# Kernel optimization log

Measured on AMD Instinct MI355X. Metric: run time of the kernel, lower is better.

The kernel has to match this reference:

```python
import jax, jax.numpy as jnp
import numpy as np

SIGMA = 0.1
B_PARAM = 1.0
EPS_NORM = 1e-12  # torch F.normalize eps
EPS_MIN = 1e-5


def setup_inputs() -> dict:
    key = jax.random.key(0)
    k1, k2 = jax.random.split(key)
    x = jax.random.normal(k1, (4, 64, 64, 64), dtype=jnp.float32)
    y = jax.random.normal(k2, (4, 64, 64, 64), dtype=jnp.float32)
    return {"x": x, "y": y}


def reference(x, y):
    B, C, H, W = x.shape
    N = H * W
    xf = x.reshape(B, C, N)
    yf = y.reshape(B, C, N)
    # F.normalize along channel dim (L2, eps-clamped denominator)
    xn = xf / jnp.maximum(jnp.linalg.norm(xf, axis=1, keepdims=True), EPS_NORM)
    yn = yf / jnp.maximum(jnp.linalg.norm(yf, axis=1, keepdims=True), EPS_NORM)
    xt = jnp.transpose(xn, (0, 2, 1))  # [B, N, C]
    yt = jnp.transpose(yn, (0, 2, 1))  # [B, N, C]
    x2 = jnp.sum(xt * xt, axis=-1, keepdims=True)          # [B, N, 1]
    y2 = jnp.sum(yt * yt, axis=-1)[:, None, :]             # [B, 1, N]
    d2 = x2 + y2 - 2.0 * jnp.einsum('bnc,bmc->bnm', xt, yt)  # [B, N, N]
    dist = jnp.sqrt(jnp.maximum(d2, 0.0))
    d_min = jnp.min(dist, axis=-1, keepdims=True)
    d_scaled = dist / (d_min + EPS_MIN)
    w = jnp.exp((B_PARAM - d_scaled) / SIGMA)
    cx = w / jnp.sum(w, axis=-1, keepdims=True)
    cx_max = jnp.max(cx, axis=-1)  # [B, N]
    return -jnp.log(jnp.mean(cx_max + EPS_MIN))
```

## Files before the change

kernel.cpp:

```cpp
#include <hip/hip_runtime.h>
#include <math.h>

constexpr int B_   = 4;
constexpr int C_   = 64;
constexpr int HW   = 4096;
constexpr int ROWS = B_ * HW;
constexpr int GRID = 256;

constexpr float SIGMA    = 0.1f;
constexpr float EPS_MIN  = 1e-5f;
constexpr float EPS_NORM = 1e-12f;
constexpr float LOG2E    = 1.44269504088896340736f;

constexpr int XR  = 64;
constexpr int NW  = 16;
constexpr int YW  = HW / NW;
constexpr int SRW = 32;
constexpr int NSW = YW / SRW;

using short8  = __attribute__((ext_vector_type(8))) short;
using floatx4 = __attribute__((ext_vector_type(4))) float;

__device__ inline ushort f2bf(float f) {
    unsigned u = __float_as_uint(f);
    unsigned r = u + 0x7FFFu + ((u >> 16) & 1u);
    return (ushort)(r >> 16);
}

__device__ inline void gload16(const ushort* g, void* lds) {
    __builtin_amdgcn_global_load_lds(
        (const __attribute__((address_space(1))) void*)g,
        (__attribute__((address_space(3))) void*)lds, 16, 0, 0);
}

#define WAIT_VMCNT(n) asm volatile("s_waitcnt vmcnt(" #n ")" ::: "memory")

__global__ __launch_bounds__(256) void nrm_kernel(const float* __restrict__ x,
                                                  const float* __restrict__ y,
                                                  ushort* __restrict__ xn,
                                                  ushort* __restrict__ yn,
                                                  float* __restrict__ total,
                                                  unsigned* __restrict__ cnt) {
    int p = blockIdx.x * 256 + threadIdx.x;
    if (p == 0) { *total = 0.0f; *cnt = 0u; }
    const float* src; ushort* dst; int q; float sgn; bool isy;
    if (p < ROWS) { src = x; dst = xn; q = p; sgn = -2.0f; isy = false; }
    else          { src = y; dst = yn; q = p - ROWS; sgn = 1.0f; isy = true; }
    int b = q >> 12;
    int n = q & (HW - 1);
    const float* base = src + (size_t)(b * C_) * HW + n;
    float v[C_];
    float ss = 0.0f;
#pragma unroll
    for (int c = 0; c < C_; ++c) {
        v[c] = base[(size_t)c * HW];
        ss = fmaf(v[c], v[c], ss);
    }
    float scale = sgn / fmaxf(sqrtf(ss), EPS_NORM);
    short8* o = (short8*)(dst + (size_t)q * C_);
    int sw = isy ? (n & 7) : 0;
#pragma unroll
    for (int c8 = 0; c8 < C_ / 8; ++c8) {
        short8 pk;
#pragma unroll
        for (int j = 0; j < 8; ++j) pk[j] = (short)f2bf(v[c8 * 8 + j] * scale);
        o[c8 ^ sw] = pk;
    }
}

__global__ __launch_bounds__(1024, 4) void main_kernel(const ushort* __restrict__ xn,
                                                       const ushort* __restrict__ yn,
                                                       float* __restrict__ total,
                                                       unsigned* __restrict__ cnt,
                                                       float* __restrict__ out) {
    __shared__ short8 stg[NW][2][SRW * 8];
    __shared__ float  red[NW][XR];
    __shared__ float  dmf[XR];

    const int tid  = threadIdx.x;
    const int wid  = tid >> 6;
    const int lane = tid & 63;
    const int lrow = lane & 15;
    const int kgrp = lane >> 4;

    const int blk   = blockIdx.x;
    const int b     = blk >> 6;
    const int nbase = (blk & 63) * XR;

    const ushort* xb = xn + (size_t)(b * HW + nbase) * C_;
    short8 xf0[4], xf1[4];
#pragma unroll
    for (int xt = 0; xt < 4; ++xt) {
        xf0[xt] = *(const short8*)(xb + (xt * 16 + lrow) * C_ + kgrp * 8);
        xf1[xt] = *(const short8*)(xb + (xt * 16 + lrow) * C_ + 32 + kgrp * 8);
    }

    const ushort* yb = yn + (size_t)(b * HW + wid * YW) * C_ + lane * 8;

#define ISSUE(s, buf) do {                                              \
        const ushort* gp_ = yb + (size_t)(s) * SRW * C_;                \
        _Pragma("unroll")                                               \
        for (int g_ = 0; g_ < 4; ++g_)                                  \
            gload16(gp_ + g_ * 64 * 8, (void*)&stg[wid][buf][g_ * 64]); \
    } while (0)

    float m2[4] = {INFINITY, INFINITY, INFINITY, INFINITY};

    ISSUE(0, 0);
    for (int s = 0; s < NSW; ++s) {
        int cur = s & 1;
        if (s + 1 < NSW) { ISSUE(s + 1, cur ^ 1); WAIT_VMCNT(4); }
        else             { WAIT_VMCNT(0); }
        __builtin_amdgcn_sched_barrier(0);
#pragma unroll
        for (int yt = 0; yt < 2; ++yt) {
            int p = yt * 16 + lrow, q = p & 7;
            short8 ya0 = stg[wid][cur][p * 8 + (kgrp ^ q)];
            short8 ya1 = stg[wid][cur][p * 8 + ((kgrp + 4) ^ q)];
#pragma unroll
            for (int xt = 0; xt < 4; ++xt) {
                floatx4 acc = {2.0f, 2.0f, 2.0f, 2.0f};
                acc = __builtin_amdgcn_mfma_f32_16x16x32_bf16(ya0, xf0[xt], acc, 0, 0, 0);
                acc = __builtin_amdgcn_mfma_f32_16x16x32_bf16(ya1, xf1[xt], acc, 0, 0, 0);
                m2[xt] = fminf(fminf(fminf(acc[0], acc[1]), acc[2]),
                               fminf(acc[3], m2[xt]));
            }
        }
    }

#pragma unroll
    for (int off = 16; off < 64; off <<= 1)
#pragma unroll
        for (int xt = 0; xt < 4; ++xt)
            m2[xt] = fminf(m2[xt], __shfl_xor(m2[xt], off));
    if (kgrp == 0)
#pragma unroll
        for (int xt = 0; xt < 4; ++xt) red[wid][xt * 16 + lrow] = m2[xt];
    __syncthreads();
    if (tid < XR) {
        float m = red[0][tid];
#pragma unroll
        for (int w = 1; w < NW; ++w) m = fminf(m, red[w][tid]);
        dmf[tid] = sqrtf(fmaxf(m, 0.0f));
    }
    __syncthreads();

    float kk2[4], c02[4];
#pragma unroll
    for (int xt = 0; xt < 4; ++xt) {
        float dm = dmf[xt * 16 + lrow];
        kk2[xt] = LOG2E / (SIGMA * (dm + EPS_MIN));
        c02[xt] = dm * kk2[xt];
    }

    float s2[4] = {0.0f, 0.0f, 0.0f, 0.0f};
    ISSUE(0, 0);
    for (int s = 0; s < NSW; ++s) {
        int cur = s & 1;
        if (s + 1 < NSW) { ISSUE(s + 1, cur ^ 1); WAIT_VMCNT(4); }
        else             { WAIT_VMCNT(0); }
        __builtin_amdgcn_sched_barrier(0);
#pragma unroll
        for (int yt = 0; yt < 2; ++yt) {
            int p = yt * 16 + lrow, q = p & 7;
            short8 ya0 = stg[wid][cur][p * 8 + (kgrp ^ q)];
            short8 ya1 = stg[wid][cur][p * 8 + ((kgrp + 4) ^ q)];
#pragma unroll
            for (int xt = 0; xt < 4; ++xt) {
                floatx4 acc = {2.0f, 2.0f, 2.0f, 2.0f};
                acc = __builtin_amdgcn_mfma_f32_16x16x32_bf16(ya0, xf0[xt], acc, 0, 0, 0);
                acc = __builtin_amdgcn_mfma_f32_16x16x32_bf16(ya1, xf1[xt], acc, 0, 0, 0);
                float d0 = __builtin_amdgcn_sqrtf(acc[0]);
                float d1 = __builtin_amdgcn_sqrtf(acc[1]);
                float d2 = __builtin_amdgcn_sqrtf(acc[2]);
                float d3 = __builtin_amdgcn_sqrtf(acc[3]);
                s2[xt] += __builtin_amdgcn_exp2f(fmaf(-kk2[xt], d0, c02[xt]));
                s2[xt] += __builtin_amdgcn_exp2f(fmaf(-kk2[xt], d1, c02[xt]));
                s2[xt] += __builtin_amdgcn_exp2f(fmaf(-kk2[xt], d2, c02[xt]));
                s2[xt] += __builtin_amdgcn_exp2f(fmaf(-kk2[xt], d3, c02[xt]));
            }
        }
    }
#undef ISSUE

#pragma unroll
    for (int off = 16; off < 64; off <<= 1)
#pragma unroll
        for (int xt = 0; xt < 4; ++xt)
            s2[xt] += __shfl_xor(s2[xt], off);
    if (kgrp == 0)
#pragma unroll
        for (int xt = 0; xt < 4; ++xt) red[wid][xt * 16 + lrow] = s2[xt];
    __syncthreads();

    if (tid < 64) {
        float Ssum = (tid < XR) ? red[0][tid] : 0.0f;
        if (tid < XR)
#pragma unroll
            for (int w = 1; w < NW; ++w) Ssum += red[w][tid];
        float acc = (tid < XR) ? (__builtin_amdgcn_rcpf(Ssum) + EPS_MIN) : 0.0f;
#pragma unroll
        for (int off = 32; off > 0; off >>= 1) acc += __shfl_down(acc, off);
        if (tid == 0) {
            atomicAdd(total, acc);
            __threadfence();
            unsigned done = atomicAdd(cnt, 1u);
            if (done == GRID - 1) {
                __threadfence();
                float t = atomicAdd(total, 0.0f);
                out[0] = -logf(t / (float)ROWS);
            }
        }
    }
}

extern "C" void kernel_launch(void* const* d_in, const int* in_sizes, int n_in,
                              void* d_out, int out_size, void* d_ws, size_t ws_size,
                              hipStream_t stream) {
    const float* x = (const float*)d_in[0];
    const float* y = (const float*)d_in[1];
    float* out = (float*)d_out;

    char* ws = (char*)d_ws;
    size_t nrm_bytes = (size_t)ROWS * C_ * sizeof(ushort);
    ushort*   xn    = (ushort*)(ws);
    ushort*   yn    = (ushort*)(ws + nrm_bytes);
    float*    total = (float*)(ws + 2 * nrm_bytes);
    unsigned* cnt   = (unsigned*)(ws + 2 * nrm_bytes + 16);

    hipLaunchKernelGGL(nrm_kernel, dim3(2 * ROWS / 256), dim3(256), 0, stream,
                       x, y, xn, yn, total, cnt);
    hipLaunchKernelGGL(main_kernel, dim3(GRID), dim3(1024), 0, stream,
                       xn, yn, total, cnt, out);
}
```

Before: 95.27 us.

## Split Y range across two blocks per X tile with separate min and sum passes

Each 64-row X tile is now handled by two blocks that each cover half of the Y columns, doubling the grid to 512 blocks. To make that possible the fused kernel is split into a min pass and a sum pass, joined through a global atomicMin array and a global atomicAdd array of per-row sums. The normalize kernel now spreads each row across two threads, and a final last-block reduction computes the loss. This aims to fill more CUs on the GPU, at the cost of two extra launches, global atomics, and a serial 16K-row final reduction in one block.

```diff
diff --git a/kernel.cpp b/kernel.cpp
--- a/kernel.cpp
+++ b/kernel.cpp
@@ -5,18 +5,19 @@
 constexpr int C_   = 64;
 constexpr int HW   = 4096;
 constexpr int ROWS = B_ * HW;
-constexpr int GRID = 256;
 
 constexpr float SIGMA    = 0.1f;
 constexpr float EPS_MIN  = 1e-5f;
 constexpr float EPS_NORM = 1e-12f;
 constexpr float LOG2E    = 1.44269504088896340736f;
 
-constexpr int XR  = 64;
-constexpr int NW  = 16;
-constexpr int YW  = HW / NW;
-constexpr int SRW = 32;
-constexpr int NSW = YW / SRW;
+constexpr int XR   = 64;
+constexpr int YH   = HW / 2;
+constexpr int NW   = 16;
+constexpr int YW   = YH / NW;
+constexpr int SRW  = 16;
+constexpr int NSW  = YW / SRW;
+constexpr int GRID = 512;
 
 using short8  = __attribute__((ext_vector_type(8))) short;
 using floatx4 = __attribute__((ext_vector_type(4))) float;
@@ -39,92 +40,90 @@
                                                   const float* __restrict__ y,
                                                   ushort* __restrict__ xn,
                                                   ushort* __restrict__ yn,
+                                                  unsigned* __restrict__ dmin_u,
                                                   float* __restrict__ total,
                                                   unsigned* __restrict__ cnt) {
-    int p = blockIdx.x * 256 + threadIdx.x;
-    if (p == 0) { *total = 0.0f; *cnt = 0u; }
-    const float* src; ushort* dst; int q; float sgn; bool isy;
-    if (p < ROWS) { src = x; dst = xn; q = p; sgn = -2.0f; isy = false; }
-    else          { src = y; dst = yn; q = p - ROWS; sgn = 1.0f; isy = true; }
+    int T = blockIdx.x * 256 + threadIdx.x;
+    if (T == 0) { *total = 0.0f; *cnt = 0u; }
+    if (T < ROWS) dmin_u[T] = 0x7F800000u;
+    int q = T >> 1;
+    int h = T & 1;
+    const float* src; ushort* dst; float sgn; bool isy;
+    if (q < ROWS) { src = x; dst = xn; sgn = -2.0f; isy = false; }
+    else          { src = y; dst = yn; q -= ROWS; sgn = 1.0f; isy = true; }
     int b = q >> 12;
     int n = q & (HW - 1);
-    const float* base = src + (size_t)(b * C_) * HW + n;
-    float v[C_];
+    const float* base = src + (size_t)(b * C_) * HW + (size_t)(h * 32) * HW + n;
+    float v[32];
     float ss = 0.0f;
 #pragma unroll
-    for (int c = 0; c < C_; ++c) {
-        v[c] = base[(size_t)c * HW];
-        ss = fmaf(v[c], v[c], ss);
-    }
+    for (int j = 0; j < 32; ++j) {
+        v[j] = base[(size_t)j * HW];
+        ss = fmaf(v[j], v[j], ss);
+    }
+    ss += __shfl_xor(ss, 1);
     float scale = sgn / fmaxf(sqrtf(ss), EPS_NORM);
-    short8* o = (short8*)(dst + (size_t)q * C_);
+    short8* orow = (short8*)(dst + (size_t)q * C_);
     int sw = isy ? (n & 7) : 0;
 #pragma unroll
-    for (int c8 = 0; c8 < C_ / 8; ++c8) {
+    for (int j4 = 0; j4 < 4; ++j4) {
         short8 pk;
 #pragma unroll
-        for (int j = 0; j < 8; ++j) pk[j] = (short)f2bf(v[c8 * 8 + j] * scale);
-        o[c8 ^ sw] = pk;
-    }
-}
-
-__global__ __launch_bounds__(1024, 4) void main_kernel(const ushort* __restrict__ xn,
-                                                       const ushort* __restrict__ yn,
-                                                       float* __restrict__ total,
-                                                       unsigned* __restrict__ cnt,
-                                                       float* __restrict__ out) {
+        for (int j = 0; j < 8; ++j) pk[j] = (short)f2bf(v[j4 * 8 + j] * scale);
+        orow[(h * 4 + j4) ^ sw] = pk;
+    }
+}
+
+#define PASS_SETUP                                                          \
+    const int tid  = threadIdx.x;                                           \
+    const int wid  = tid >> 6;                                   \
+    const int lane = tid & 63;                                              \
+    const int lrow = lane & 15;                      \
+    const int kgrp = lane >> 4;                           \
+    const int pairid = blockIdx.x >> 1;                                     \
+    const int half   = blockIdx.x & 1;                                      \
+    const int b      = pairid >> 6;                 \
+    const int nbase  = (pairid & 63) * XR;                                  \
+    const ushort* xb = xn + (size_t)(b * HW + nbase) * C_;                  \
+    short8 xf0[4], xf1[4];                                                  \
+    _Pragma("unroll")                                                       \
+    for (int xt = 0; xt < 4; ++xt) {                                        \
+        xf0[xt] = *(const short8*)(xb + (xt * 16 + lrow) * C_ + kgrp * 8);  \
+        xf1[xt] = *(const short8*)(xb + (xt * 16 + lrow) * C_ + 32 + kgrp * 8); \
+    }                                                                       \
+    const ushort* yb = yn + (size_t)(b * HW + half * YH + wid * YW) * C_    \
+                          + lane * 8;
+
+#define ISSUE(s, buf) do {                                              \
+        const ushort* gp_ = yb + (size_t)(s) * SRW * C_;                \
+        gload16(gp_,           (void*)&stg[wid][buf][0]);               \
+        gload16(gp_ + 64 * 8,  (void*)&stg[wid][buf][64]);              \
+    } while (0)
+
+__global__ __launch_bounds__(1024, 8) void pass1_kernel(const ushort* __restrict__ xn,
+                                                        const ushort* __restrict__ yn,
+                                                        unsigned* __restrict__ dmin_u) {
     __shared__ short8 stg[NW][2][SRW * 8];
     __shared__ float  red[NW][XR];
-    __shared__ float  dmf[XR];
-
-    const int tid  = threadIdx.x;
-    const int wid  = tid >> 6;
-    const int lane = tid & 63;
-    const int lrow = lane & 15;
-    const int kgrp = lane >> 4;
-
-    const int blk   = blockIdx.x;
-    const int b     = blk >> 6;
-    const int nbase = (blk & 63) * XR;
-
-    const ushort* xb = xn + (size_t)(b * HW + nbase) * C_;
-    short8 xf0[4], xf1[4];
-#pragma unroll
-    for (int xt = 0; xt < 4; ++xt) {
-        xf0[xt] = *(const short8*)(xb + (xt * 16 + lrow) * C_ + kgrp * 8);
-        xf1[xt] = *(const short8*)(xb + (xt * 16 + lrow) * C_ + 32 + kgrp * 8);
-    }
-
-    const ushort* yb = yn + (size_t)(b * HW + wid * YW) * C_ + lane * 8;
-
-#define ISSUE(s, buf) do {                                              \
-        const ushort* gp_ = yb + (size_t)(s) * SRW * C_;                \
-        _Pragma("unroll")                                               \
-        for (int g_ = 0; g_ < 4; ++g_)                                  \
-            gload16(gp_ + g_ * 64 * 8, (void*)&stg[wid][buf][g_ * 64]); \
-    } while (0)
+    PASS_SETUP
 
     float m2[4] = {INFINITY, INFINITY, INFINITY, INFINITY};
-
     ISSUE(0, 0);
     for (int s = 0; s < NSW; ++s) {
         int cur = s & 1;
-        if (s + 1 < NSW) { ISSUE(s + 1, cur ^ 1); WAIT_VMCNT(4); }
+        if (s + 1 < NSW) { ISSUE(s + 1, cur ^ 1); WAIT_VMCNT(2); }
         else             { WAIT_VMCNT(0); }
         __builtin_amdgcn_sched_barrier(0);
-#pragma unroll
-        for (int yt = 0; yt < 2; ++yt) {
-            int p = yt * 16 + lrow, q = p & 7;
-            short8 ya0 = stg[wid][cur][p * 8 + (kgrp ^ q)];
-            short8 ya1 = stg[wid][cur][p * 8 + ((kgrp + 4) ^ q)];
-#pragma unroll
-            for (int xt = 0; xt < 4; ++xt) {
-                floatx4 acc = {2.0f, 2.0f, 2.0f, 2.0f};
-                acc = __builtin_amdgcn_mfma_f32_16x16x32_bf16(ya0, xf0[xt], acc, 0, 0, 0);
-                acc = __builtin_amdgcn_mfma_f32_16x16x32_bf16(ya1, xf1[xt], acc, 0, 0, 0);
-                m2[xt] = fminf(fminf(fminf(acc[0], acc[1]), acc[2]),
-                               fminf(acc[3], m2[xt]));
-            }
+        int p = lrow, q = p & 7;
+        short8 ya0 = stg[wid][cur][p * 8 + (kgrp ^ q)];
+        short8 ya1 = stg[wid][cur][p * 8 + ((kgrp + 4) ^ q)];
+#pragma unroll
+        for (int xt = 0; xt < 4; ++xt) {
+            floatx4 acc = {2.0f, 2.0f, 2.0f, 2.0f};
+            acc = __builtin_amdgcn_mfma_f32_16x16x32_bf16(ya0, xf0[xt], acc, 0, 0, 0);
+            acc = __builtin_amdgcn_mfma_f32_16x16x32_bf16(ya1, xf1[xt], acc, 0, 0, 0);
+            m2[xt] = fminf(fminf(fminf(acc[0], acc[1]), acc[2]),
+                           fminf(acc[3], m2[xt]));
         }
     }
 
@@ -141,14 +140,25 @@
         float m = red[0][tid];
 #pragma unroll
         for (int w = 1; w < NW; ++w) m = fminf(m, red[w][tid]);
-        dmf[tid] = sqrtf(fmaxf(m, 0.0f));
-    }
-    __syncthreads();
+        float d = sqrtf(fmaxf(m, 0.0f));
+        atomicMin(&dmin_u[b * HW + nbase + tid], __float_as_uint(d));
+    }
+}
+
+__global__ __launch_bounds__(1024, 8) void pass2_kernel(const ushort* __restrict__ xn,
+                                                        const ushort* __restrict__ yn,
+                                                        const unsigned* __restrict__ dmin_u,
+                                                        float* __restrict__ Sacc,
+                                                        unsigned* __restrict__ cnt,
+                                                        float* __restrict__ out) {
+    __shared__ short8 stg[NW][2][SRW * 8];
+    __shared__ float  red[NW][XR];
+    PASS_SETUP
 
     float kk2[4], c02[4];
 #pragma unroll
     for (int xt = 0; xt < 4; ++xt) {
-        float dm = dmf[xt * 16 + lrow];
+        float dm = __uint_as_float(dmin_u[b * HW + nbase + xt * 16 + lrow]);
         kk2[xt] = LOG2E / (SIGMA * (dm + EPS_MIN));
         c02[xt] = dm * kk2[xt];
     }
@@ -157,31 +167,27 @@
     ISSUE(0, 0);
     for (int s = 0; s < NSW; ++s) {
         int cur = s & 1;
-        if (s + 1 < NSW) { ISSUE(s + 1, cur ^ 1); WAIT_VMCNT(4); }
+        if (s + 1 < NSW) { ISSUE(s + 1, cur ^ 1); WAIT_VMCNT(2); }
         else             { WAIT_VMCNT(0); }
         __builtin_amdgcn_sched_barrier(0);
-#pragma unroll
-        for (int yt = 0; yt < 2; ++yt) {
-            int p = yt * 16 + lrow, q = p & 7;
-            short8 ya0 = stg[wid][cur][p * 8 + (kgrp ^ q)];
-            short8 ya1 = stg[wid][cur][p * 8 + ((kgrp + 4) ^ q)];
-#pragma unroll
-            for (int xt = 0; xt < 4; ++xt) {
-                floatx4 acc = {2.0f, 2.0f, 2.0f, 2.0f};
-                acc = __builtin_amdgcn_mfma_f32_16x16x32_bf16(ya0, xf0[xt], acc, 0, 0, 0);
-                acc = __builtin_amdgcn_mfma_f32_16x16x32_bf16(ya1, xf1[xt], acc, 0, 0, 0);
-                float d0 = __builtin_amdgcn_sqrtf(acc[0]);
-                float d1 = __builtin_amdgcn_sqrtf(acc[1]);
-                float d2 = __builtin_amdgcn_sqrtf(acc[2]);
-                float d3 = __builtin_amdgcn_sqrtf(acc[3]);
-                s2[xt] += __builtin_amdgcn_exp2f(fmaf(-kk2[xt], d0, c02[xt]));
-                s2[xt] += __builtin_amdgcn_exp2f(fmaf(-kk2[xt], d1, c02[xt]));
-                s2[xt] += __builtin_amdgcn_exp2f(fmaf(-kk2[xt], d2, c02[xt]));
-                s2[xt] += __builtin_amdgcn_exp2f(fmaf(-kk2[xt], d3, c02[xt]));
-            }
+        int p = lrow, q = p & 7;
+        short8 ya0 = stg[wid][cur][p * 8 + (kgrp ^ q)];
+        short8 ya1 = stg[wid][cur][p * 8 + ((kgrp + 4) ^ q)];
+#pragma unroll
+        for (int xt = 0; xt < 4; ++xt) {
+            floatx4 acc = {2.0f, 2.0f, 2.0f, 2.0f};
+            acc = __builtin_amdgcn_mfma_f32_16x16x32_bf16(ya0, xf0[xt], acc, 0, 0, 0);
+            acc = __builtin_amdgcn_mfma_f32_16x16x32_bf16(ya1, xf1[xt], acc, 0, 0, 0);
+            float d0 = __builtin_amdgcn_sqrtf(acc[0]);
+            float d1 = __builtin_amdgcn_sqrtf(acc[1]);
+            float d2 = __builtin_amdgcn_sqrtf(acc[2]);
+            float d3 = __builtin_amdgcn_sqrtf(acc[3]);
+            s2[xt] += __builtin_amdgcn_exp2f(fmaf(-kk2[xt], d0, c02[xt]));
+            s2[xt] += __builtin_amdgcn_exp2f(fmaf(-kk2[xt], d1, c02[xt]));
+            s2[xt] += __builtin_amdgcn_exp2f(fmaf(-kk2[xt], d2, c02[xt]));
+            s2[xt] += __builtin_amdgcn_exp2f(fmaf(-kk2[xt], d3, c02[xt]));
         }
     }
-#undef ISSUE
 
 #pragma unroll
     for (int off = 16; off < 64; off <<= 1)
@@ -193,25 +199,43 @@
         for (int xt = 0; xt < 4; ++xt) red[wid][xt * 16 + lrow] = s2[xt];
     __syncthreads();
 
-    if (tid < 64) {
-        float Ssum = (tid < XR) ? red[0][tid] : 0.0f;
-        if (tid < XR)
-#pragma unroll
-            for (int w = 1; w < NW; ++w) Ssum += red[w][tid];
-        float acc = (tid < XR) ? (__builtin_amdgcn_rcpf(Ssum) + EPS_MIN) : 0.0f;
+    if (tid < XR) {
+        float Ssum = red[0][tid];
+#pragma unroll
+        for (int w = 1; w < NW; ++w) Ssum += red[w][tid];
+        atomicAdd(&Sacc[b * HW + nbase + tid], Ssum);
+    }
+    __syncthreads();
+
+    if (tid == 0) {
+        __threadfence();
+        if (atomicAdd(cnt, 1u) == GRID - 1) *cnt = 0xFFFFFFFFu;
+    }
+    __syncthreads();
+    __threadfence();
+    if (*((volatile unsigned*)cnt) == 0xFFFFFFFFu) {
+        __shared__ float fin[NW];
+        float acc = 0.0f;
+        for (int i = tid; i < ROWS; i += 1024)
+            acc += __builtin_amdgcn_rcpf(Sacc[i]) + EPS_MIN;
 #pragma unroll
         for (int off = 32; off > 0; off >>= 1) acc += __shfl_down(acc, off);
+        if (lane == 0) fin[wid] = acc;
+        __syncthreads();
         if (tid == 0) {
-            atomicAdd(total, acc);
-            __threadfence();
-            unsigned done = atomicAdd(cnt, 1u);
-            if (done == GRID - 1) {
-                __threadfence();
-                float t = atomicAdd(total, 0.0f);
-                out[0] = -logf(t / (float)ROWS);
-            }
+            float t = 0.0f;
+#pragma unroll
+            for (int w = 0; w < NW; ++w) t += fin[w];
+            out[0] = -logf(t / (float)ROWS);
         }
     }
+}
+#undef ISSUE
+#undef PASS_SETUP
+
+__global__ __launch_bounds__(256) void zs_kernel(float* __restrict__ Sacc) {
+    int i = blockIdx.x * 256 + threadIdx.x;
+    if (i < ROWS) Sacc[i] = 0.0f;
 }
 
 extern "C" void kernel_launch(void* const* d_in, const int* in_sizes, int n_in,
@@ -225,11 +249,16 @@
     size_t nrm_bytes = (size_t)ROWS * C_ * sizeof(ushort);
     ushort*   xn    = (ushort*)(ws);
     ushort*   yn    = (ushort*)(ws + nrm_bytes);
-    float*    total = (float*)(ws + 2 * nrm_bytes);
-    unsigned* cnt   = (unsigned*)(ws + 2 * nrm_bytes + 16);
-
-    hipLaunchKernelGGL(nrm_kernel, dim3(2 * ROWS / 256), dim3(256), 0, stream,
-                       x, y, xn, yn, total, cnt);
-    hipLaunchKernelGGL(main_kernel, dim3(GRID), dim3(1024), 0, stream,
-                       xn, yn, total, cnt, out);
-}
+    unsigned* dmin_u = (unsigned*)(ws + 2 * nrm_bytes);
+    float*    Sacc   = (float*)(ws + 2 * nrm_bytes + ROWS * sizeof(unsigned));
+    float*    total  = (float*)(ws + 2 * nrm_bytes + ROWS * 8);
+    unsigned* cnt    = (unsigned*)(ws + 2 * nrm_bytes + ROWS * 8 + 16);
+
+    hipLaunchKernelGGL(zs_kernel, dim3(ROWS / 256), dim3(256), 0, stream, Sacc);
+    hipLaunchKernelGGL(nrm_kernel, dim3(4 * ROWS / 256), dim3(256), 0, stream,
+                       x, y, xn, yn, dmin_u, total, cnt);
+    hipLaunchKernelGGL(pass1_kernel, dim3(GRID), dim3(1024), 0, stream,
+                       xn, yn, dmin_u);
+    hipLaunchKernelGGL(pass2_kernel, dim3(GRID), dim3(1024), 0, stream,
+                       xn, yn, dmin_u, Sacc, cnt, out);
+}
```

Measured after the change: 318.3 us. 3.34x slower.
